# Kernel tuning notes

Measured on AMD Instinct MI355X. Metric: run time of the kernel, lower is better.

The kernel has to match this reference:

```python
import jax, jax.numpy as jnp
import numpy as np

B, T, H, DK, DV = 4, 2048, 1024, 1024, 1024


def setup_inputs() -> dict:
    key = jax.random.key(0)
    ks = jax.random.split(key, 9)
    s = lambda fan_in: 1.0 / np.sqrt(fan_in)
    return {
        "y_all": jax.random.normal(ks[0], (B, T, H), dtype=jnp.float32),
        "Wq": jax.random.uniform(ks[1], (H, DK), jnp.float32, -s(H), s(H)),
        "bq": jax.random.uniform(ks[2], (DK,), jnp.float32, -s(H), s(H)),
        "Wk": jax.random.uniform(ks[3], (H, DK), jnp.float32, -s(H), s(H)),
        "bk": jax.random.uniform(ks[4], (DK,), jnp.float32, -s(H), s(H)),
        "Wv": jax.random.uniform(ks[5], (H, DV), jnp.float32, -s(H), s(H)),
        "bv": jax.random.uniform(ks[6], (DV,), jnp.float32, -s(H), s(H)),
        "Wo": jax.random.uniform(ks[7], (DV, H), jnp.float32, -s(DV), s(DV)),
        "bo": jax.random.uniform(ks[8], (H,), jnp.float32, -s(DV), s(DV)),
    }


def reference(y_all, Wq, bq, Wk, bk, Wv, bv, Wo, bo):
    # Fused causal attention equivalent to the per-timestep Python loop.
    dk = Wq.shape[1]
    q = (y_all @ Wq + bq) / jnp.sqrt(jnp.asarray(dk, y_all.dtype))  # [B,T,DK]
    k = y_all @ Wk + bk                                             # [B,T,DK]
    v = y_all @ Wv + bv                                             # [B,T,DV]
    scores = jnp.einsum("bqd,bkd->bqk", q, k)                       # [B,T,T]
    t = y_all.shape[1]
    causal = jnp.tril(jnp.ones((t, t), dtype=bool))                 # [T,T]
    scores = jnp.where(causal[None], scores, jnp.asarray(-jnp.inf, scores.dtype))
    w = jax.nn.softmax(scores, axis=-1)                             # [B,T,T]
    ctx = jnp.einsum("bqk,bkd->bqd", w, v)                          # [B,T,DV]
    return ctx @ Wo + bo                                            # [B,T,H]
```

## Files before the change

kernel.cpp:

```cpp
#include <hip/hip_runtime.h>
#include <hip/hip_bf16.h>
#include <cstdint>

#define DEVI __device__ __forceinline__

typedef __attribute__((ext_vector_type(8))) short bf16x8;
typedef __attribute__((ext_vector_type(4))) short bf16x4;
typedef __attribute__((ext_vector_type(4))) float f32x4;

DEVI short f2bf(float f) {
  unsigned u = __float_as_uint(f);
  u += 0x7fff + ((u >> 16) & 1);
  return (short)(u >> 16);
}
DEVI float bf2f(short s) { return __uint_as_float(((unsigned)(unsigned short)s) << 16); }

DEVI void gl_lds16(const short* g, short* l) {
  __builtin_amdgcn_global_load_lds((const __attribute__((address_space(1))) unsigned*)g,
                                   (__attribute__((address_space(3))) unsigned*)l, 16, 0, 0);
}

constexpr int BM = 128, BN = 128, BK = 64;

template<int MODE, int BIASMODE, bool OUTF32, int DECODE>
__global__ __launch_bounds__(256, 2)
void gemm_bt(const short* __restrict__ A, const short* __restrict__ B,
             void* __restrict__ Cv, const float* __restrict__ b0,
             float scale, int K, int lda, int ldb, int ldc,
             long long sA, long long sB, long long sC, int tdim)
{
  const int nwg = gridDim.x, orig = blockIdx.x;
  const int q8 = nwg >> 3, r8 = nwg & 7;
  const int xcd = orig & 7, idx8 = orig >> 3;
  const int wg = (xcd < r8 ? xcd * (q8 + 1) : r8 * (q8 + 1) + (xcd - r8) * q8) + idx8;
  const int bz = blockIdx.z;

  int bi, bj;
  if constexpr (MODE == 4) {
    int b = (int)((__fsqrt_rn(8.f * (float)wg + 1.f) - 1.f) * 0.5f);
    if ((b + 1) * (b + 2) / 2 <= wg) ++b;
    if (b * (b + 1) / 2 > wg) --b;
    bi = b; bj = wg - b * (b + 1) / 2;
  } else {
    bi = wg / tdim;
    bj = wg - bi * tdim;
    if constexpr (DECODE == 3) { if (bz & 2) bi = (nwg / tdim) - 1 - bi; }
  }

  A += (long long)bz * sA;
  B += (long long)bz * sB;

  __shared__ __align__(16) short lA[2][BM * BK];
  __shared__ __align__(16) short lB[2][BN * BK];

  const int tid = threadIdx.x, wave = tid >> 6, lane = tid & 63;
  const int wr = wave >> 1, wc = wave & 1;
  const int brow = bi * BM, bcol = bj * BN;
  const int fr = lane & 15, h = lane >> 4;

  const int ck0 = ((h ^ (fr & 7))) * 8;
  const int swc = ((tid & 7) ^ ((tid >> 3) & 7)) * 8;
  const short* pA = A + (long long)(brow + (tid >> 3)) * lda + swc;
  const short* pB = B + (long long)(bcol + (tid >> 3)) * ldb + swc;

  f32x4 acc[4][4] = {};
  const int kend = (MODE == 2) ? (bi + 1) * BM : K;
  const int nt = kend / BK;

  auto stage = [&](int buf, int t) {
    const long long ko = (long long)t * BK;
#pragma unroll
    for (int j = 0; j < 4; ++j)
      gl_lds16(pA + (long long)(j * 32) * lda + ko, &lA[buf][j * 2048 + tid * 8]);
#pragma unroll
    for (int j = 0; j < 4; ++j)
      gl_lds16(pB + (long long)(j * 32) * ldb + ko, &lB[buf][j * 2048 + tid * 8]);
  };

  stage(0, 0);
  __syncthreads();

  int cur = 0;
  for (int t = 0; t < nt; ++t) {
    if (t + 1 < nt) stage(cur ^ 1, t + 1);

    const short* bufA = lA[cur];
    const short* bufB = lB[cur];
    bf16x8 af[4], bg[4];
#pragma unroll
    for (int m = 0; m < 4; ++m)
      af[m] = *(const bf16x8*)&bufA[(wr * 64 + m * 16 + fr) * BK + ck0];
#pragma unroll
    for (int n = 0; n < 4; ++n)
      bg[n] = *(const bf16x8*)&bufB[(wc * 64 + n * 16 + fr) * BK + ck0];
#pragma unroll
    for (int m = 0; m < 4; ++m)
#pragma unroll
      for (int n = 0; n < 4; ++n)
        acc[m][n] = __builtin_amdgcn_mfma_f32_16x16x32_bf16(af[m], bg[n], acc[m][n], 0, 0, 0);
#pragma unroll
    for (int m = 0; m < 4; ++m)
      af[m] = *(const bf16x8*)&bufA[((wr * 64 + m * 16 + fr) * BK + ck0) ^ 32];
#pragma unroll
    for (int n = 0; n < 4; ++n)
      bg[n] = *(const bf16x8*)&bufB[((wc * 64 + n * 16 + fr) * BK + ck0) ^ 32];
#pragma unroll
    for (int m = 0; m < 4; ++m)
#pragma unroll
      for (int n = 0; n < 4; ++n)
        acc[m][n] = __builtin_amdgcn_mfma_f32_16x16x32_bf16(af[m], bg[n], acc[m][n], 0, 0, 0);

    __syncthreads();
    cur ^= 1;
  }

  const int lrow = h * 4;
  float* Cf = (float*)Cv + (long long)bz * sC;
  short* Cs = (short*)Cv + (long long)bz * sC;
  int colg[4]; float bvv[4];
#pragma unroll
  for (int n = 0; n < 4; ++n) {
    colg[n] = bcol + wc * 64 + n * 16 + fr;
    bvv[n] = (BIASMODE == 1) ? b0[colg[n]] : 0.f;
  }
#pragma unroll
  for (int m = 0; m < 4; ++m) {
    const int row = brow + wr * 64 + m * 16 + lrow;
#pragma unroll
    for (int j = 0; j < 4; ++j) {
#pragma unroll
      for (int n = 0; n < 4; ++n) {
        const float val = (acc[m][n][j] + bvv[n]) * scale;
        if constexpr (OUTF32) Cf[(long long)(row + j) * ldc + colg[n]] = val;
        else                  Cs[(long long)(row + j) * ldc + colg[n]] = f2bf(val);
      }
    }
  }
}

__global__ __launch_bounds__(256, 4)
void gemm_g(const short* __restrict__ ybf, const short* __restrict__ MTb,
            short* __restrict__ G, const float* __restrict__ wvec)
{
  const int orig = blockIdx.x;
  const int xcd = orig & 7, idx8 = orig >> 3;
  const int wg = xcd * 64 + idx8;
  const int bi = wg >> 3, bj = wg & 7;

  __shared__ __align__(16) short lA[BM * BK];
  __shared__ __align__(16) short lB[BN * BK];

  const int tid = threadIdx.x, wave = tid >> 6, lane = tid & 63;
  const int wr = wave >> 1, wc = wave & 1;
  const int brow = bi * BM, bcol = bj * BN;
  const int fr = lane & 15, h = lane >> 4;

  const int ck0 = ((h ^ (fr & 7))) * 8;
  const int swc = ((tid & 7) ^ ((tid >> 3) & 7)) * 8;
  const short* pA = ybf + (long long)(brow + (tid >> 3)) * 1024 + swc;
  const short* pB = MTb + (long long)(bcol + (tid >> 3)) * 1024 + swc;

  f32x4 acc[4][4] = {};

  for (int t = 0; t < 16; ++t) {
    const long long ko = (long long)t * BK;
#pragma unroll
    for (int j = 0; j < 4; ++j)
      gl_lds16(pA + (long long)(j * 32) * 1024 + ko, &lA[j * 2048 + tid * 8]);
#pragma unroll
    for (int j = 0; j < 4; ++j)
      gl_lds16(pB + (long long)(j * 32) * 1024 + ko, &lB[j * 2048 + tid * 8]);
    __syncthreads();

    bf16x8 af[4], bg[4];
#pragma unroll
    for (int m = 0; m < 4; ++m)
      af[m] = *(const bf16x8*)&lA[(wr * 64 + m * 16 + fr) * BK + ck0];
#pragma unroll
    for (int n = 0; n < 4; ++n)
      bg[n] = *(const bf16x8*)&lB[(wc * 64 + n * 16 + fr) * BK + ck0];
#pragma unroll
    for (int m = 0; m < 4; ++m)
#pragma unroll
      for (int n = 0; n < 4; ++n)
        acc[m][n] = __builtin_amdgcn_mfma_f32_16x16x32_bf16(af[m], bg[n], acc[m][n], 0, 0, 0);
#pragma unroll
    for (int m = 0; m < 4; ++m)
      af[m] = *(const bf16x8*)&lA[((wr * 64 + m * 16 + fr) * BK + ck0) ^ 32];
#pragma unroll
    for (int n = 0; n < 4; ++n)
      bg[n] = *(const bf16x8*)&lB[((wc * 64 + n * 16 + fr) * BK + ck0) ^ 32];
#pragma unroll
    for (int m = 0; m < 4; ++m)
#pragma unroll
      for (int n = 0; n < 4; ++n)
        acc[m][n] = __builtin_amdgcn_mfma_f32_16x16x32_bf16(af[m], bg[n], acc[m][n], 0, 0, 0);
    __syncthreads();
  }

  const int lrow = h * 4;
  int colg[4]; float bvv[4];
#pragma unroll
  for (int n = 0; n < 4; ++n) {
    colg[n] = bcol + wc * 64 + n * 16 + fr;
    bvv[n] = wvec[colg[n]];
  }
#pragma unroll
  for (int m = 0; m < 4; ++m) {
    const int row = brow + wr * 64 + m * 16 + lrow;
#pragma unroll
    for (int j = 0; j < 4; ++j)
#pragma unroll
      for (int n = 0; n < 4; ++n)
        G[(long long)(row + j) * 1024 + colg[n]] =
            f2bf((acc[m][n][j] + bvv[n]) * (1.f / 32.f));
  }
}

__global__ __launch_bounds__(256, 4)
void gemm_sz(const short* __restrict__ G, const short* __restrict__ ybf,
             const short* __restrict__ WvoT, short* __restrict__ scores,
             short* __restrict__ zT)
{
  const int orig = blockIdx.x;
  const int xcd = orig & 7, idx8 = orig >> 3;
  const int wg = xcd * 132 + idx8;

  const short *A, *B; short* C; int ldc, bi, bj;
  if (wg < 544) {
    const int z = wg / 136, t = wg - z * 136;
    int b = (int)((__fsqrt_rn(8.f * (float)t + 1.f) - 1.f) * 0.5f);
    if ((b + 1) * (b + 2) / 2 <= t) ++b;
    if (b * (b + 1) / 2 > t) --b;
    bi = b; bj = t - b * (b + 1) / 2;
    A = G + (long long)z * 2048 * 1024;
    B = ybf + (long long)z * 2048 * 1024;
    C = scores + (long long)z * 2048 * 2048;
    ldc = 2048;
  } else {
    const int lwg = wg - 544;
    bi = lwg >> 6; bj = lwg & 63;
    A = WvoT; B = ybf; C = zT; ldc = 8192;
  }

  __shared__ __align__(16) short lA[BM * BK];
  __shared__ __align__(16) short lB[BN * BK];

  const int tid = threadIdx.x, wave = tid >> 6, lane = tid & 63;
  const int wr = wave >> 1, wc = wave & 1;
  const int brow = bi * BM, bcol = bj * BN;
  const int fr = lane & 15, h = lane >> 4;

  const int ck0 = ((h ^ (fr & 7))) * 8;
  const int swc = ((tid & 7) ^ ((tid >> 3) & 7)) * 8;
  const short* pA = A + (long long)(brow + (tid >> 3)) * 1024 + swc;
  const short* pB = B + (long long)(bcol + (tid >> 3)) * 1024 + swc;

  f32x4 acc[4][4] = {};

  for (int t = 0; t < 16; ++t) {
    const long long ko = (long long)t * BK;
#pragma unroll
    for (int j = 0; j < 4; ++j)
      gl_lds16(pA + (long long)(j * 32) * 1024 + ko, &lA[j * 2048 + tid * 8]);
#pragma unroll
    for (int j = 0; j < 4; ++j)
      gl_lds16(pB + (long long)(j * 32) * 1024 + ko, &lB[j * 2048 + tid * 8]);
    __syncthreads();

    bf16x8 af[4], bg[4];
#pragma unroll
    for (int m = 0; m < 4; ++m)
      af[m] = *(const bf16x8*)&lA[(wr * 64 + m * 16 + fr) * BK + ck0];
#pragma unroll
    for (int n = 0; n < 4; ++n)
      bg[n] = *(const bf16x8*)&lB[(wc * 64 + n * 16 + fr) * BK + ck0];
#pragma unroll
    for (int m = 0; m < 4; ++m)
#pragma unroll
      for (int n = 0; n < 4; ++n)
        acc[m][n] = __builtin_amdgcn_mfma_f32_16x16x32_bf16(af[m], bg[n], acc[m][n], 0, 0, 0);
#pragma unroll
    for (int m = 0; m < 4; ++m)
      af[m] = *(const bf16x8*)&lA[((wr * 64 + m * 16 + fr) * BK + ck0) ^ 32];
#pragma unroll
    for (int n = 0; n < 4; ++n)
      bg[n] = *(const bf16x8*)&lB[((wc * 64 + n * 16 + fr) * BK + ck0) ^ 32];
#pragma unroll
    for (int m = 0; m < 4; ++m)
#pragma unroll
      for (int n = 0; n < 4; ++n)
        acc[m][n] = __builtin_amdgcn_mfma_f32_16x16x32_bf16(af[m], bg[n], acc[m][n], 0, 0, 0);
    __syncthreads();
  }

  const int lrow = h * 4;
  int colg[4];
#pragma unroll
  for (int n = 0; n < 4; ++n) colg[n] = bcol + wc * 64 + n * 16 + fr;
#pragma unroll
  for (int m = 0; m < 4; ++m) {
    const int row = brow + wr * 64 + m * 16 + lrow;
#pragma unroll
    for (int j = 0; j < 4; ++j)
#pragma unroll
      for (int n = 0; n < 4; ++n)
        C[(long long)(row + j) * ldc + colg[n]] = f2bf(acc[m][n][j]);
  }
}

__global__ __launch_bounds__(256)
void softmax_causal_bf16_k(short* __restrict__ sc)
{
  const int T = 2048;
  const long long row = blockIdx.x;
  const int t = (int)(row & (T - 1));
  short* ps = sc + row * (long long)T;
  const int tid = threadIdx.x, wave = tid >> 6, lane = tid & 63;
  const int c0 = tid * 8;
  const int wlim = ((t >> 7) + 1) << 7;

  bf16x8 v = {};
  if (c0 <= t) v = *(const bf16x8*)&ps[c0];
  float x[8];
#pragma unroll
  for (int j = 0; j < 8; ++j) x[j] = bf2f(v[j]);

  float mx = -3.0e38f;
#pragma unroll
  for (int j = 0; j < 8; ++j) if (c0 + j <= t) mx = fmaxf(mx, x[j]);
#pragma unroll
  for (int o = 32; o; o >>= 1) mx = fmaxf(mx, __shfl_xor(mx, o, 64));
  __shared__ float red[8];
  if (lane == 0) red[wave] = mx;
  __syncthreads();
  const float M = fmaxf(fmaxf(red[0], red[1]), fmaxf(red[2], red[3]));

  float e[8], s = 0.f;
#pragma unroll
  for (int j = 0; j < 8; ++j) { e[j] = (c0 + j <= t) ? __expf(x[j] - M) : 0.f; s += e[j]; }
#pragma unroll
  for (int o = 32; o; o >>= 1) s += __shfl_xor(s, o, 64);
  if (lane == 0) red[4 + wave] = s;
  __syncthreads();
  const float inv = 1.f / (red[4] + red[5] + red[6] + red[7]);

  if (c0 < wlim) {
    bf16x8 ov;
#pragma unroll
    for (int j = 0; j < 8; ++j) ov[j] = f2bf(e[j] * inv);
    *(bf16x8*)&ps[c0] = ov;
  }
}

__global__ __launch_bounds__(256)
void cvt_y_k(const float* __restrict__ y, short* __restrict__ ybf)
{
  const long long i = (long long)blockIdx.x * 256 + threadIdx.x;
  const float4 v0 = ((const float4*)y)[i * 2];
  const float4 v1 = ((const float4*)y)[i * 2 + 1];
  bf16x8 o;
  o[0] = f2bf(v0.x); o[1] = f2bf(v0.y); o[2] = f2bf(v0.z); o[3] = f2bf(v0.w);
  o[4] = f2bf(v1.x); o[5] = f2bf(v1.y); o[6] = f2bf(v1.z); o[7] = f2bf(v1.w);
  ((bf16x8*)ybf)[i] = o;
}

__global__ __launch_bounds__(256)
void cvt_w_all_k(const float* __restrict__ w0, const float* __restrict__ w1,
                 const float* __restrict__ w2, const float* __restrict__ w3,
                 short* __restrict__ o0, short* __restrict__ o1,
                 short* __restrict__ o2, short* __restrict__ o3)
{
  const int tx = threadIdx.x & 31, ty = threadIdx.x >> 5;
  const int r0 = blockIdx.y * 32, c0 = blockIdx.x * 32;
  if (blockIdx.z != 2) {
    const float* in = (blockIdx.z == 0) ? w0 : (blockIdx.z == 1 ? w1 : w3);
    short* out      = (blockIdx.z == 0) ? o0 : (blockIdx.z == 1 ? o1 : o3);
#pragma unroll
    for (int i = 0; i < 4; ++i)
      out[(long long)(r0 + ty + 8 * i) * 1024 + c0 + tx] =
          f2bf(in[(long long)(r0 + ty + 8 * i) * 1024 + c0 + tx]);
    return;
  }
  __shared__ float tile[32][33];
#pragma unroll
  for (int i = 0; i < 4; ++i)
    tile[ty + 8 * i][tx] = w2[(long long)(r0 + ty + 8 * i) * 1024 + c0 + tx];
  __syncthreads();
#pragma unroll
  for (int i = 0; i < 4; ++i)
    o2[(long long)(c0 + ty + 8 * i) * 1024 + r0 + tx] = f2bf(tile[tx][ty + 8 * i]);
}

__global__ __launch_bounds__(256)
void bias_init_k(const float* __restrict__ bo, float* __restrict__ outb)
{
  const int j = blockIdx.x * 256 + threadIdx.x;
  outb[j] = bo[j];
}

__global__ __launch_bounds__(256)
void bias_fold_k(const float* __restrict__ bv, const float* __restrict__ Wo,
                 float* __restrict__ outb)
{
  const int r0 = blockIdx.x * 16;
  const int c4 = threadIdx.x;
  float4 acc = make_float4(0.f, 0.f, 0.f, 0.f);
  for (int r = 0; r < 16; ++r) {
    const float s = bv[r0 + r];
    const float4 w = ((const float4*)(Wo + (long long)(r0 + r) * 1024))[c4];
    acc.x += s * w.x; acc.y += s * w.y; acc.z += s * w.z; acc.w += s * w.w;
  }
  atomicAdd(&outb[c4 * 4 + 0], acc.x);
  atomicAdd(&outb[c4 * 4 + 1], acc.y);
  atomicAdd(&outb[c4 * 4 + 2], acc.z);
  atomicAdd(&outb[c4 * 4 + 3], acc.w);
}

__global__ __launch_bounds__(256)
void wkbq_gemv_k(const float* __restrict__ Wk, const float* __restrict__ bq,
                 float* __restrict__ w)
{
  const int row = blockIdx.x, tid = threadIdx.x;
  const float4 a = ((const float4*)(Wk + (long long)row * 1024))[tid];
  const float4 b = ((const float4*)bq)[tid];
  float s = a.x * b.x + a.y * b.y + a.z * b.z + a.w * b.w;
#pragma unroll
  for (int o = 32; o; o >>= 1) s += __shfl_xor(s, o, 64);
  __shared__ float red[4];
  if ((tid & 63) == 0) red[tid >> 6] = s;
  __syncthreads();
  if (tid == 0) w[row] = red[0] + red[1] + red[2] + red[3];
}

__global__ __launch_bounds__(256)
void combine4_k(const float* __restrict__ p, short* __restrict__ out)
{
  const long long i = (long long)blockIdx.x * 256 + threadIdx.x;
  const float4 a = ((const float4*)p)[i];
  const float4 b = ((const float4*)(p + 1048576))[i];
  const float4 c = ((const float4*)(p + 2097152))[i];
  const float4 d = ((const float4*)(p + 3145728))[i];
  bf16x4 o;
  o[0] = f2bf(a.x + b.x + c.x + d.x);
  o[1] = f2bf(a.y + b.y + c.y + d.y);
  o[2] = f2bf(a.z + b.z + c.z + d.z);
  o[3] = f2bf(a.w + b.w + c.w + d.w);
  ((bf16x4*)out)[i] = o;
}

extern "C" void kernel_launch(void* const* d_in, const int* in_sizes, int n_in,
                              void* d_out, int out_size, void* d_ws, size_t ws_size,
                              hipStream_t stream)
{
  (void)in_sizes; (void)n_in; (void)out_size; (void)ws_size;
  const float* y  = (const float*)d_in[0];
  const float* Wq = (const float*)d_in[1];
  const float* bq = (const float*)d_in[2];
  const float* Wk = (const float*)d_in[3];
  const float* bk = (const float*)d_in[4];
  const float* Wv = (const float*)d_in[5];
  const float* bv = (const float*)d_in[6];
  const float* Wo = (const float*)d_in[7];
  const float* bo = (const float*)d_in[8];
  float* out = (float*)d_out;
  (void)bk;

  const int T = 2048;
  const long long MT = 8192;
  const long long MM = 1048576;

  short* ws    = (short*)d_ws;
  short* ybf   = ws;
  short* WqBf  = ybf + MT * 1024;
  short* WkBf  = WqBf + MM;
  short* WoT   = WkBf + MM;
  short* WvBf  = WoT + MM;
  short* MTb   = WvBf + MM;
  short* WvoT  = MTb + MM;
  short* G     = WvoT + MM;
  short* zT    = G + MT * 1024;
  short* scores = zT + MT * 1024;
  float* bvWoBo = (float*)(scores + 4ll * T * T);
  float* wvec   = bvWoBo + 1024;
  float* part   = wvec + 1024;

  cvt_y_k<<<4096, 256, 0, stream>>>(y, ybf);
  cvt_w_all_k<<<dim3(32, 32, 4), 256, 0, stream>>>(
      Wq, Wk, Wo, Wv, WqBf, WkBf, WoT, WvBf);
  bias_init_k<<<4, 256, 0, stream>>>(bo, bvWoBo);
  bias_fold_k<<<64, 256, 0, stream>>>(bv, Wo, bvWoBo);
  wkbq_gemv_k<<<1024, 256, 0, stream>>>(Wk, bq, wvec);

  gemm_bt<0, 0, true, 0><<<dim3(64, 1, 4), 256, 0, stream>>>(
      WkBf, WqBf, part, nullptr, 1.f, 256, 1024, 1024, 1024,
      256, 256, 1048576, 8);
  combine4_k<<<1024, 256, 0, stream>>>(part, MTb);

  gemm_bt<0, 0, true, 0><<<dim3(64, 1, 4), 256, 0, stream>>>(
      WoT, WvBf, part, nullptr, 1.f, 256, 1024, 1024, 1024,
      256, 256, 1048576, 8);
  combine4_k<<<1024, 256, 0, stream>>>(part, WvoT);

  gemm_g<<<512, 256, 0, stream>>>(ybf, MTb, G, wvec);

  gemm_sz<<<1056, 256, 0, stream>>>(G, ybf, WvoT, scores, zT);

  softmax_causal_bf16_k<<<(int)MT, 256, 0, stream>>>(scores);

  gemm_bt<2, 1, true, 3><<<dim3(16 * 8, 1, 4), 256, 0, stream>>>(
      scores, zT, out, bvWoBo, 1.f, T, T, 8192, 1024,
      (long long)T * T, 2048, 2048ll * 1024, 8);
}
```

Measured before the change: 180.0 us.

## Replace final causal PV GEMM with 64x64-tile kernel and finer causal softmax bound

Adds a dedicated gemm_pv kernel for the final causal scores×zT product. It uses 64x64 tiles with a K-loop limited to the causal extent, and maps blocks so each XCD handles one batch and tile parity. It replaces the 128x128 gemm_bt MODE 2 launch, which had a load imbalance across triangular tiles, with many smaller blocks at higher occupancy. The softmax zero-fill limit is tightened to 64-column granularity to match the new tile size, and the now-unused MODE 2/4 decode paths are removed from gemm_bt. The new kernel is single-buffered with a sync per tile, so it loses the load/compute overlap the old kernel had.

Result: faster. 175.3 us (-2.6%).

```diff
diff --git a/kernel.cpp b/kernel.cpp
--- a/kernel.cpp
+++ b/kernel.cpp
@@ -35,17 +35,8 @@
   const int wg = (xcd < r8 ? xcd * (q8 + 1) : r8 * (q8 + 1) + (xcd - r8) * q8) + idx8;
   const int bz = blockIdx.z;
 
-  int bi, bj;
-  if constexpr (MODE == 4) {
-    int b = (int)((__fsqrt_rn(8.f * (float)wg + 1.f) - 1.f) * 0.5f);
-    if ((b + 1) * (b + 2) / 2 <= wg) ++b;
-    if (b * (b + 1) / 2 > wg) --b;
-    bi = b; bj = wg - b * (b + 1) / 2;
-  } else {
-    bi = wg / tdim;
-    bj = wg - bi * tdim;
-    if constexpr (DECODE == 3) { if (bz & 2) bi = (nwg / tdim) - 1 - bi; }
-  }
+  int bi = wg / tdim;
+  const int bj = wg - bi * tdim;
 
   A += (long long)bz * sA;
   B += (long long)bz * sB;
@@ -64,8 +55,7 @@
   const short* pB = B + (long long)(bcol + (tid >> 3)) * ldb + swc;
 
   f32x4 acc[4][4] = {};
-  const int kend = (MODE == 2) ? (bi + 1) * BM : K;
-  const int nt = kend / BK;
+  const int nt = K / BK;
 
   auto stage = [&](int buf, int t) {
     const long long ko = (long long)t * BK;
@@ -309,6 +299,88 @@
   }
 }
 
+__global__ __launch_bounds__(256, 6)
+void gemm_pv(const short* __restrict__ scores, const short* __restrict__ zT,
+             float* __restrict__ out, const float* __restrict__ bias)
+{
+  const int orig = blockIdx.x;
+  const int xcd = orig & 7, idx8 = orig >> 3;
+  const int z = xcd >> 1;
+  const int bi = ((idx8 >> 4) << 1) | (xcd & 1);
+  const int bj = idx8 & 15;
+
+  const short* A = scores + (long long)z * 2048 * 2048;
+  const int nt = bi + 1;
+
+  __shared__ __align__(16) short lA[64 * 64];
+  __shared__ __align__(16) short lB[64 * 64];
+
+  const int tid = threadIdx.x, wave = tid >> 6, lane = tid & 63;
+  const int wm = wave >> 1, wn = wave & 1;
+  const int brow = bi * 64, bcol = bj * 64;
+  const int fr = lane & 15, h = lane >> 4;
+
+  const int ck0 = ((h ^ (fr & 7))) * 8;
+  const int swc = ((tid & 7) ^ ((tid >> 3) & 7)) * 8;
+  const short* pA = A + (long long)(brow + (tid >> 3)) * 2048 + swc;
+  const short* pB = zT + (long long)(bcol + (tid >> 3)) * 8192 + z * 2048 + swc;
+
+  f32x4 acc[2][2] = {};
+
+  for (int t = 0; t < nt; ++t) {
+    const long long ko = (long long)t * 64;
+#pragma unroll
+    for (int j = 0; j < 2; ++j)
+      gl_lds16(pA + (long long)(j * 32) * 2048 + ko, &lA[j * 2048 + tid * 8]);
+#pragma unroll
+    for (int j = 0; j < 2; ++j)
+      gl_lds16(pB + (long long)(j * 32) * 8192 + ko, &lB[j * 2048 + tid * 8]);
+    __syncthreads();
+
+    bf16x8 af[2], bg[2];
+#pragma unroll
+    for (int m = 0; m < 2; ++m)
+      af[m] = *(const bf16x8*)&lA[(wm * 32 + m * 16 + fr) * 64 + ck0];
+#pragma unroll
+    for (int n = 0; n < 2; ++n)
+      bg[n] = *(const bf16x8*)&lB[(wn * 32 + n * 16 + fr) * 64 + ck0];
+#pragma unroll
+    for (int m = 0; m < 2; ++m)
+#pragma unroll
+      for (int n = 0; n < 2; ++n)
+        acc[m][n] = __builtin_amdgcn_mfma_f32_16x16x32_bf16(af[m], bg[n], acc[m][n], 0, 0, 0);
+#pragma unroll
+    for (int m = 0; m < 2; ++m)
+      af[m] = *(const bf16x8*)&lA[((wm * 32 + m * 16 + fr) * 64 + ck0) ^ 32];
+#pragma unroll
+    for (int n = 0; n < 2; ++n)
+      bg[n] = *(const bf16x8*)&lB[((wn * 32 + n * 16 + fr) * 64 + ck0) ^ 32];
+#pragma unroll
+    for (int m = 0; m < 2; ++m)
+#pragma unroll
+      for (int n = 0; n < 2; ++n)
+        acc[m][n] = __builtin_amdgcn_mfma_f32_16x16x32_bf16(af[m], bg[n], acc[m][n], 0, 0, 0);
+    __syncthreads();
+  }
+
+  const int lrow = h * 4;
+  int colg[2]; float bvv[2];
+#pragma unroll
+  for (int n = 0; n < 2; ++n) {
+    colg[n] = bcol + wn * 32 + n * 16 + fr;
+    bvv[n] = bias[colg[n]];
+  }
+#pragma unroll
+  for (int m = 0; m < 2; ++m) {
+    const int row = brow + wm * 32 + m * 16 + lrow;
+#pragma unroll
+    for (int j = 0; j < 4; ++j)
+#pragma unroll
+      for (int n = 0; n < 2; ++n)
+        out[(long long)(z * 2048 + row + j) * 1024 + colg[n]] = acc[m][n][j] + bvv[n];
+  }
+}
+
 __global__ __launch_bounds__(256)
 void softmax_causal_bf16_k(short* __restrict__ sc)
 {
@@ -318,7 +390,7 @@
   short* ps = sc + row * (long long)T;
   const int tid = threadIdx.x, wave = tid >> 6, lane = tid & 63;
   const int c0 = tid * 8;
-  const int wlim = ((t >> 7) + 1) << 7;
+  const int wlim = ((t >> 6) + 1) << 6;
 
   bf16x8 v = {};
   if (c0 <= t) v = *(const bf16x8*)&ps[c0];
@@ -508,7 +580,5 @@
 
   softmax_causal_bf16_k<<<(int)MT, 256, 0, stream>>>(scores);
 
-  gemm_bt<2, 1, true, 3><<<dim3(16 * 8, 1, 4), 256, 0, stream>>>(
-      scores, zT, out, bvWoBo, 1.f, T, T, 8192, 1024,
-      (long long)T * T, 2048, 2048ll * 1024, 8);
-}
+  gemm_pv<<<2048, 256, 0, stream>>>(scores, zT, out, bvWoBo);
+}
```
